# Optimization experiments

Hardware: AMD Instinct MI355X
Metric: run time of the kernel (lower is better)

The kernel has to match this reference:

```python
import jax, jax.numpy as jnp
import numpy as np

# Standard SMPL kinematic tree parents (kintree_table)
PARENTS = np.array([-1, 0, 0, 0, 1, 2, 3, 4, 5, 6, 7, 8, 9, 9, 9,
                    12, 13, 14, 16, 17, 18, 19, 20, 21])
NV, NJ, NB, NP = 6890, 24, 10, 207


def rodrigues(r):
    """Axis-angle [N,3] -> rotation matrices [N,3,3] (Rodrigues formula)."""
    theta = jnp.linalg.norm(r, axis=1, keepdims=True) + 1e-8  # [N,1]
    rh = r / theta                                            # [N,3]
    cos = jnp.cos(theta)[..., None]                           # [N,1,1]
    sin = jnp.sin(theta)[..., None]
    z = jnp.zeros_like(rh[:, 0])
    m = jnp.stack([z, -rh[:, 2], rh[:, 1],
                   rh[:, 2], z, -rh[:, 0],
                   -rh[:, 1], rh[:, 0], z], axis=1).reshape(-1, 3, 3)
    dot = rh[:, :, None] * rh[:, None, :]                     # outer product
    eye = jnp.eye(3, dtype=r.dtype)
    return cos * eye + (1.0 - cos) * dot + sin * m


def setup_inputs() -> dict:
    key = jax.random.key(0)
    ks = jax.random.split(key, 9)
    B = 512
    betas = jax.random.normal(ks[0], (B, NB), dtype=jnp.float32)
    thetas = jax.random.normal(ks[1], (B, NJ * 3), dtype=jnp.float32) * 0.3
    trans = jax.random.normal(ks[2], (B, 3), dtype=jnp.float32)
    scale = jnp.ones((1,), dtype=jnp.float32)
    v_template = jax.random.normal(ks[3], (NV, 3), dtype=jnp.float32)
    shapedirs = jax.random.normal(ks[4], (NV, 3, NB), dtype=jnp.float32) * 0.01
    posedirs = jax.random.normal(ks[5], (NV, 3, NP), dtype=jnp.float32) * 0.01
    Jr = jax.random.uniform(ks[6], (NJ, NV), dtype=jnp.float32)
    J_regressor = Jr / jnp.sum(Jr, axis=1, keepdims=True)
    w = jax.random.uniform(ks[7], (NV, NJ), dtype=jnp.float32)
    weights = w / jnp.sum(w, axis=1, keepdims=True)
    return {"betas": betas, "thetas": thetas, "trans": trans, "scale": scale,
            "v_template": v_template, "shapedirs": shapedirs,
            "posedirs": posedirs, "J_regressor": J_regressor,
            "weights": weights}


def reference(betas, thetas, trans, scale, v_template, shapedirs, posedirs,
              J_regressor, weights):
    B = betas.shape[0]
    dt = betas.dtype
    # Shape blend shapes: v_shaped [B, 6890, 3]
    v_shaped = jnp.einsum('bs,vcs->bvc', betas, shapedirs) + v_template
    # Rest-pose joints J(beta): [B, 24, 3]
    J = jnp.einsum('jv,bvc->bjc', J_regressor, v_shaped)
    # Local rotations from axis-angle, root scaled by `scale`
    lRs = rodrigues(thetas.reshape(-1, 3)).reshape(B, NJ, 3, 3)
    lRs = lRs.at[:, 0].multiply(scale[0])
    # Local joint offsets: root keeps J[:,0], children use J[i] - J[parent[i]]
    parents = jnp.asarray(PARENTS)
    t = J - J[:, jnp.clip(parents, 0)]
    t = t.at[:, 0].set(J[:, 0])
    # Local 4x4 transforms [B, 24, 4, 4]
    top = jnp.concatenate([lRs, t[..., None]], axis=3)          # [B,24,3,4]
    bottom = jnp.broadcast_to(jnp.array([0., 0., 0., 1.], dtype=dt),
                              (B, NJ, 1, 4))
    A = jnp.concatenate([top, bottom], axis=2)
    # Kinematic chain accumulation (fixed 24-joint tree)
    results = [A[:, 0]]
    for i in range(1, NJ):
        results.append(results[PARENTS[i]] @ A[:, i])
    stacked = jnp.stack(results, axis=1)                         # [B,24,4,4]
    # Remove rest-pose joint locations from translation column
    Jh = jnp.concatenate([J, jnp.zeros((B, NJ, 1), dtype=dt)], axis=2)
    deformed = jnp.einsum('bjxy,bjy->bjx', stacked, Jh)          # [B,24,4]
    G = stacked.at[..., 3].add(-deformed)
    # Pose blend shapes from non-root rotations
    lrotmin = (lRs[:, 1:] - jnp.eye(3, dtype=dt)).reshape(B, -1)  # [B,207]
    v_posed = v_shaped + jnp.einsum('bp,vcp->bvc', lrotmin, posedirs)
    # Linear blend skinning
    T = jnp.einsum('bjxy,vj->bvxy', G, weights)                  # [B,6890,4,4]
    vh = jnp.concatenate([v_posed, jnp.ones((B, NV, 1), dtype=dt)], axis=2)
    v = jnp.einsum('bvxy,bvy->bvx', T, vh)[:, :, :3]
    result = v + trans[:, None, :]
    joints = jnp.einsum('jv,bvc->bjc', J_regressor, result)
    return result, joints
```

## Files before the change

kernel.cpp:

```cpp
#include <hip/hip_runtime.h>

#define NVERT 6890
#define NJNT  24
#define NBETA 10
#define NPOSE 207
#define NBATCH 512
#define KPAD 224
#define MROWS 20736
#define NVC (NVERT * 3)

typedef __attribute__((ext_vector_type(8))) short short8;
typedef __attribute__((ext_vector_type(4))) float floatx4;

__constant__ int c_par[NJNT]   = {-1,0,0,0,1,2,3,4,5,6,7,8,9,9,9,12,13,14,16,17,18,19,20,21};
__constant__ int c_depth[NJNT] = { 0,1,1,1,2,2,2,3,3,3,4,4,4,4,4,5,5,5,6,6,7,7,8,8};

static __device__ __forceinline__ unsigned short f2bf(float x) {
  union { float f; unsigned u; } v; v.f = x;
  unsigned r = (v.u + 0x7FFFu + ((v.u >> 16) & 1u)) >> 16;
  return (unsigned short)r;
}
static __device__ __forceinline__ float bf2f(unsigned short h) {
  union { unsigned u; float f; } v; v.u = (unsigned)h << 16;
  return v.f;
}

__global__ __launch_bounds__(256) void k_buildA(
    const float* __restrict__ pdir, const float* __restrict__ sd,
    const float* __restrict__ vt, unsigned short* __restrict__ AT) {
  const int idx = blockIdx.x * 256 + threadIdx.x;
  const int row = idx / KPAD, k = idx - row * KPAD;
  float val = 0.f;
  if (row < NVC) {
    if (k < NPOSE)            val = pdir[(size_t)row * NPOSE + k];
    else if (k < NPOSE + 10)  val = sd[(size_t)row * 10 + (k - NPOSE)];
    else if (k == NPOSE + 10) val = vt[row];
  }
  AT[idx] = f2bf(val);
}

__global__ __launch_bounds__(256) void k_buildW(
    const float* __restrict__ wgt, unsigned short* __restrict__ W16) {
  const int idx = blockIdx.x * 256 + threadIdx.x;
  const int v = idx >> 6, c = idx & 63, j = c & 31, h = c >> 5;
  const float w = (v < NVERT && j < 24) ? wgt[(size_t)v * 24 + j] : 0.f;
  const unsigned short hi = f2bf(w);
  W16[idx] = h ? f2bf(w - bf2f(hi)) : hi;
}

__global__ __launch_bounds__(256) void k_jreg1(
    const float* __restrict__ Jr, const float* __restrict__ vt,
    const float* __restrict__ sd, float* __restrict__ wsJP) {
  const int jc = blockIdx.x, j = jc / 3, c = jc % 3;
  const int v0 = blockIdx.y * 864;
  const int vend = min(NVERT, v0 + 864);
  const int tid = threadIdx.x;
  float acc[11];
  #pragma unroll
  for (int k = 0; k < 11; ++k) acc[k] = 0.f;
  for (int v = v0 + tid; v < vend; v += 256) {
    const float w = Jr[j * NVERT + v];
    acc[0] += w * vt[v * 3 + c];
    const float* s = sd + (size_t)v * 30 + c * 10;
    #pragma unroll
    for (int k = 0; k < 10; ++k) acc[1 + k] += w * s[k];
  }
  #pragma unroll
  for (int off = 32; off > 0; off >>= 1) {
    #pragma unroll
    for (int k = 0; k < 11; ++k) acc[k] += __shfl_down(acc[k], off, 64);
  }
  __shared__ float red[4][11];
  const int lane = tid & 63, wv = tid >> 6;
  if (lane == 0) {
    #pragma unroll
    for (int k = 0; k < 11; ++k) red[wv][k] = acc[k];
  }
  __syncthreads();
  if (tid == 0) {
    #pragma unroll
    for (int k = 0; k < 11; ++k)
      wsJP[(size_t)(blockIdx.y * 72 + jc) * 11 + k] =
          red[0][k] + red[1][k] + red[2][k] + red[3][k];
  }
}

__global__ __launch_bounds__(256, 2) void k_chain3(
    const float* __restrict__ betas, const float* __restrict__ thetas,
    const float* __restrict__ scale, const float* __restrict__ trans,
    const float* __restrict__ wsJP,
    unsigned short* __restrict__ BT, unsigned short* __restrict__ G16) {
  __shared__ __align__(16) float sJ[792];
  __shared__ __align__(16) float sJJ[4][72];
  __shared__ __align__(16) float sM[4][288];
  __shared__ __align__(16) unsigned short sG[4][1024];
  __shared__ __align__(16) unsigned short sB[4][KPAD];

  const int tid = threadIdx.x;
  const int wv = tid >> 6, lane = tid & 63;
  const int b = blockIdx.x * 4 + wv;

  if (tid < 72) {
    #pragma unroll
    for (int k = 0; k < 11; ++k) {
      float s = 0.f;
      #pragma unroll
      for (int c8 = 0; c8 < 8; ++c8) s += wsJP[(size_t)(c8 * 72 + tid) * 11 + k];
      if (k == 0) sJ[tid] = s;
      else        sJ[72 + tid * 10 + (k - 1)] = s;
    }
  }
  #pragma unroll
  for (int r = 0; r < 4; ++r) {
    sG[wv][lane * 16 + r * 4 + 0] = 0; sG[wv][lane * 16 + r * 4 + 1] = 0;
    sG[wv][lane * 16 + r * 4 + 2] = 0; sG[wv][lane * 16 + r * 4 + 3] = 0;
  }
  __syncthreads();

  float R[9], t[3], M[12], Jx = 0.f, Jy = 0.f, Jz = 0.f;
  const int i = lane;
  if (i < NJNT) {
    #pragma unroll
    for (int c = 0; c < 3; ++c) {
      float a = sJ[i * 3 + c];
      const float* d = sJ + 72 + (i * 3 + c) * 10;
      #pragma unroll
      for (int s = 0; s < NBETA; ++s) a += d[s] * betas[b * NBETA + s];
      if (c == 0) Jx = a; else if (c == 1) Jy = a; else Jz = a;
    }
    sJJ[wv][i * 3 + 0] = Jx; sJJ[wv][i * 3 + 1] = Jy; sJJ[wv][i * 3 + 2] = Jz;
    const float rx = thetas[b * 72 + i * 3 + 0];
    const float ry = thetas[b * 72 + i * 3 + 1];
    const float rz = thetas[b * 72 + i * 3 + 2];
    const float th = sqrtf(rx * rx + ry * ry + rz * rz) + 1e-8f;
    const float inv = 1.f / th;
    const float x = rx * inv, y = ry * inv, z = rz * inv;
    const float cs = cosf(th), sn = sinf(th), omc = 1.f - cs;
    R[0] = cs + omc * x * x;     R[1] = omc * x * y - sn * z; R[2] = omc * x * z + sn * y;
    R[3] = omc * x * y + sn * z; R[4] = cs + omc * y * y;     R[5] = omc * y * z - sn * x;
    R[6] = omc * x * z - sn * y; R[7] = omc * y * z + sn * x; R[8] = cs + omc * z * z;
    if (i == 0) {
      const float sc = scale[0];
      #pragma unroll
      for (int k = 0; k < 9; ++k) R[k] *= sc;
    } else {
      #pragma unroll
      for (int k = 0; k < 9; ++k)
        sB[wv][(i - 1) * 9 + k] = f2bf(R[k] - ((k == 0 || k == 4 || k == 8) ? 1.f : 0.f));
    }
  }
  if (i == 0) {
    #pragma unroll
    for (int s = 0; s < NBETA; ++s) sB[wv][NPOSE + s] = f2bf(betas[b * NBETA + s]);
    sB[wv][NPOSE + 10] = 0x3F80;
    #pragma unroll
    for (int k = NPOSE + 11; k < KPAD; ++k) sB[wv][k] = 0;
  }
  __syncthreads();

  if (i < NJNT) {
    if (i == 0) { t[0] = Jx; t[1] = Jy; t[2] = Jz; }
    else {
      const int p = c_par[i];
      t[0] = Jx - sJJ[wv][p * 3 + 0];
      t[1] = Jy - sJJ[wv][p * 3 + 1];
      t[2] = Jz - sJJ[wv][p * 3 + 2];
    }
    if (i == 0) {
      #pragma unroll
      for (int r = 0; r < 3; ++r) {
        M[r*4+0] = R[r*3+0]; M[r*4+1] = R[r*3+1]; M[r*4+2] = R[r*3+2]; M[r*4+3] = t[r];
      }
      #pragma unroll
      for (int k = 0; k < 12; ++k) sM[wv][k] = M[k];
    }
  }
  __syncthreads();

  for (int lvl = 1; lvl <= 8; ++lvl) {
    if (i < NJNT && c_depth[i] == lvl) {
      const float* Mp = sM[wv] + c_par[i] * 12;
      #pragma unroll
      for (int r = 0; r < 3; ++r) {
        const float p0 = Mp[r*4+0], p1 = Mp[r*4+1], p2 = Mp[r*4+2], p3 = Mp[r*4+3];
        M[r*4+0] = p0*R[0] + p1*R[3] + p2*R[6];
        M[r*4+1] = p0*R[1] + p1*R[4] + p2*R[7];
        M[r*4+2] = p0*R[2] + p1*R[5] + p2*R[8];
        M[r*4+3] = p0*t[0] + p1*t[1] + p2*t[2] + p3;
      }
      #pragma unroll
      for (int k = 0; k < 12; ++k) sM[wv][i * 12 + k] = M[k];
    }
    __syncthreads();
  }

  if (i < NJNT) {
    #pragma unroll
    for (int r = 0; r < 3; ++r) {
      M[r*4+3] = M[r*4+3] - (M[r*4+0]*Jx + M[r*4+1]*Jy + M[r*4+2]*Jz)
               + trans[b * 3 + r];
    }
    #pragma unroll
    for (int e = 0; e < 12; ++e) {
      const float g = M[e];
      const unsigned short hi = f2bf(g);
      sG[wv][e * 32 + i]       = hi;
      sG[wv][512 + e * 32 + i] = f2bf(g - bf2f(hi));
    }
  }
  __syncthreads();

  *(uint4*)(G16 + (size_t)b * 1024 + lane * 16)     = *(uint4*)&sG[wv][lane * 16];
  *(uint4*)(G16 + (size_t)b * 1024 + lane * 16 + 8) = *(uint4*)&sG[wv][lane * 16 + 8];
  if (lane < 28)
    *(uint4*)(BT + (size_t)b * KPAD + lane * 8) = *(uint4*)&sB[wv][lane * 8];
}

__global__ __launch_bounds__(256, 3) void k_skin4(
    const unsigned short* __restrict__ AT, const unsigned short* __restrict__ BT,
    const unsigned short* __restrict__ W16, const unsigned short* __restrict__ G16,
    float* __restrict__ out) {
  __shared__ __align__(16) char smem[43776];
  unsigned short* sAs = (unsigned short*)smem;
  unsigned short* sBs = (unsigned short*)(smem + 15360);
  float* sV           = (float*)smem;
  unsigned short* sG2 = (unsigned short*)(smem + 13056);
  unsigned short* sWh = (unsigned short*)(smem + 33536);
  unsigned short* sWl = (unsigned short*)(smem + 38656);

  const int tid = threadIdx.x;
  const int wv = tid >> 6, lane = tid & 63;
  const int q = lane >> 4, n = lane & 15;
  const int b0 = blockIdx.x * 64;
  const int vc0 = blockIdx.y * 192;

  for (int i = tid; i < 512; i += 256) {
    const int row = i >> 3, c8 = i & 7;
    const uint4 w = *(const uint4*)(W16 + (size_t)(blockIdx.y * 64 + row) * 64 + c8 * 8);
    if (c8 < 4) *(uint4*)(sWh + row * 40 + c8 * 8) = w;
    else        *(uint4*)(sWl + row * 40 + (c8 - 4) * 8) = w;
  }

  floatx4 acc[3][4];
  #pragma unroll
  for (int mt = 0; mt < 3; ++mt)
    #pragma unroll
    for (int nt = 0; nt < 4; ++nt) acc[mt][nt] = (floatx4)(0.f);

  const int srow = tid >> 2, sj = tid & 3;
  for (int kt = 0; kt < 7; ++kt) {
    if (kt) __syncthreads();
    #pragma unroll
    for (int it = 0; it < 3; ++it) {
      const int row = it * 64 + srow;
      *(uint4*)(sAs + row * 40 + sj * 8) =
          *(const uint4*)(AT + (size_t)(vc0 + row) * KPAD + kt * 32 + sj * 8);
    }
    *(uint4*)(sBs + srow * 40 + sj * 8) =
        *(const uint4*)(BT + (size_t)(b0 + srow) * KPAD + kt * 32 + sj * 8);
    __syncthreads();
    short8 af[3], bfr[4];
    #pragma unroll
    for (int mt = 0; mt < 3; ++mt)
      af[mt] = *(const short8*)(sAs + (48 * wv + 16 * mt + n) * 40 + q * 8);
    #pragma unroll
    for (int nt = 0; nt < 4; ++nt)
      bfr[nt] = *(const short8*)(sBs + (16 * nt + n) * 40 + q * 8);
    #pragma unroll
    for (int mt = 0; mt < 3; ++mt)
      #pragma unroll
      for (int nt = 0; nt < 4; ++nt)
        acc[mt][nt] = __builtin_amdgcn_mfma_f32_16x16x32_bf16(
            af[mt], bfr[nt], acc[mt][nt], 0, 0, 0);
  }

  short8 wh[4], wl[4];
  #pragma unroll
  for (int vt = 0; vt < 4; ++vt) {
    wh[vt] = *(const short8*)(sWh + (vt * 16 + n) * 40 + q * 8);
    wl[vt] = *(const short8*)(sWl + (vt * 16 + n) * 40 + q * 8);
  }

  for (int nt = 0; nt < 4; ++nt) {
    for (int s = 0; s < 2; ++s) {
      __syncthreads();
      if (s == 0) {
        #pragma unroll
        for (int mt = 0; mt < 3; ++mt)
          #pragma unroll
          for (int r = 0; r < 4; ++r)
            sV[(48 * wv + 16 * mt + 4 * q + r) * 17 + n] = acc[mt][nt][r];
      }
      const int bg0 = b0 + nt * 16 + s * 8;
      for (int i = tid; i < 1024; i += 256) {
        const int row = i >> 2, c4 = i & 3;
        const int t = row >> 5, rem = row & 31;
        *(uint4*)(sG2 + row * 40 + c4 * 8) =
            *(const uint4*)(G16 + (size_t)(bg0 + t) * 1024 + rem * 32 + c4 * 8);
      }
      __syncthreads();
      #pragma unroll
      for (int bb = 0; bb < 2; ++bb) {
        const int t = wv * 2 + bb;
        const int col = s * 8 + t;
        const int bg = b0 + nt * 16 + col;
        const short8 gh = *(const short8*)(sG2 + (t * 32 + n) * 40 + q * 8);
        const short8 gl = *(const short8*)(sG2 + (t * 32 + 16 + n) * 40 + q * 8);
        #pragma unroll
        for (int vt = 0; vt < 4; ++vt) {
          floatx4 a2 = (floatx4)(0.f);
          a2 = __builtin_amdgcn_mfma_f32_16x16x32_bf16(gh, wl[vt], a2, 0, 0, 0);
          a2 = __builtin_amdgcn_mfma_f32_16x16x32_bf16(gl, wh[vt], a2, 0, 0, 0);
          a2 = __builtin_amdgcn_mfma_f32_16x16x32_bf16(gh, wh[vt], a2, 0, 0, 0);
          const float X = sV[(48 * vt + 3 * n + 0) * 17 + col];
          const float Y = sV[(48 * vt + 3 * n + 1) * 17 + col];
          const float Z = sV[(48 * vt + 3 * n + 2) * 17 + col];
          const float o = a2[0] * X + a2[1] * Y + a2[2] * Z + a2[3];
          const int vc = vc0 + 48 * vt + 3 * n + q;
          if (q < 3 && vc < NVC)
            out[(size_t)bg * NVC + vc] = o;
        }
      }
    }
  }
}

__global__ __launch_bounds__(256) void k_joints(
    const float* __restrict__ Jr, const float* __restrict__ res,
    float* __restrict__ joints) {
  const int b = blockIdx.x;
  const int lane = threadIdx.x & 63, wv = threadIdx.x >> 6;
  float acc[18];
  #pragma unroll
  for (int k = 0; k < 18; ++k) acc[k] = 0.f;
  const float* rb = res + (size_t)b * NVC;
  for (int v = lane; v < NVERT; v += 64) {
    const float r0 = rb[v*3+0], r1 = rb[v*3+1], r2 = rb[v*3+2];
    #pragma unroll
    for (int k = 0; k < 6; ++k) {
      const int j = wv + 4 * k;
      const float w = Jr[j * NVERT + v];
      acc[k*3+0] += w * r0; acc[k*3+1] += w * r1; acc[k*3+2] += w * r2;
    }
  }
  #pragma unroll
  for (int off = 32; off > 0; off >>= 1) {
    #pragma unroll
    for (int k = 0; k < 18; ++k) acc[k] += __shfl_down(acc[k], off, 64);
  }
  if (lane == 0) {
    #pragma unroll
    for (int k = 0; k < 6; ++k) {
      const int j = wv + 4 * k;
      joints[(size_t)b * 72 + j * 3 + 0] = acc[k*3+0];
      joints[(size_t)b * 72 + j * 3 + 1] = acc[k*3+1];
      joints[(size_t)b * 72 + j * 3 + 2] = acc[k*3+2];
    }
  }
}

extern "C" void kernel_launch(void* const* d_in, const int* in_sizes, int n_in,
                              void* d_out, int out_size, void* d_ws, size_t ws_size,
                              hipStream_t stream) {
  const float* betas  = (const float*)d_in[0];
  const float* thetas = (const float*)d_in[1];
  const float* trans  = (const float*)d_in[2];
  const float* scale  = (const float*)d_in[3];
  const float* vtpl   = (const float*)d_in[4];
  const float* sd     = (const float*)d_in[5];
  const float* pdir   = (const float*)d_in[6];
  const float* Jr     = (const float*)d_in[7];
  const float* wgt    = (const float*)d_in[8];
  float* out = (float*)d_out;

  float* ws   = (float*)d_ws;
  float* wsJP = ws;
  unsigned short* AT  = (unsigned short*)(ws + 6336);
  unsigned short* BT  = AT + (size_t)MROWS * KPAD;
  unsigned short* W16 = BT + (size_t)NBATCH * KPAD;
  unsigned short* G16 = W16 + (size_t)6912 * 64;

  k_buildA<<<(MROWS * KPAD) / 256, 256, 0, stream>>>(pdir, sd, vtpl, AT);
  k_buildW<<<(6912 * 64) / 256, 256, 0, stream>>>(wgt, W16);
  k_jreg1<<<dim3(72, 8), 256, 0, stream>>>(Jr, vtpl, sd, wsJP);
  k_chain3<<<NBATCH / 4, 256, 0, stream>>>(betas, thetas, scale, trans, wsJP, BT, G16);
  k_skin4<<<dim3(8, 108), 256, 0, stream>>>(AT, BT, W16, G16, out);
  k_joints<<<NBATCH, 256, 0, stream>>>(Jr, out, out + (size_t)NBATCH * NVC);
}
```

Before: 204.9 us.

## Fuse all stages into one cooperative persistent kernel with grid syncs

Replaces the six separate kernel launches with a single cooperative kernel of 256 blocks that runs the four phases (precompute, kinematic chain, skinning GEMM, joint regression) separated by grid-wide syncs. It also removes the two-level joint-regressor partial reduction, since each of 72 blocks now reduces over all vertices, and vectorises the bf16 conversion stores. The aim is to cut launch and inter-kernel gap overhead. In exchange, phase 3 runs on a fixed grid of 256 blocks looping over 864 tiles, phase 2 uses only 128 blocks, and the 72-block regressor reduction is serial over 6890 vertices. A fallback path launches the phases as separate kernels if the cooperative launch fails.

```diff
diff --git a/kernel.cpp b/kernel.cpp
--- a/kernel.cpp
+++ b/kernel.cpp
@@ -1,4 +1,7 @@
 #include <hip/hip_runtime.h>
+#include <hip/hip_cooperative_groups.h>
+
+namespace cg = cooperative_groups;
 
 #define NVERT 6890
 #define NJNT  24
@@ -8,6 +11,7 @@
 #define KPAD 224
 #define MROWS 20736
 #define NVC (NVERT * 3)
+#define GRID 256
 
 typedef __attribute__((ext_vector_type(8))) short short8;
 typedef __attribute__((ext_vector_type(4))) float floatx4;
@@ -25,96 +29,98 @@
   return v.f;
 }
 
-__global__ __launch_bounds__(256) void k_buildA(
-    const float* __restrict__ pdir, const float* __restrict__ sd,
-    const float* __restrict__ vt, unsigned short* __restrict__ AT) {
-  const int idx = blockIdx.x * 256 + threadIdx.x;
-  const int row = idx / KPAD, k = idx - row * KPAD;
-  float val = 0.f;
-  if (row < NVC) {
-    if (k < NPOSE)            val = pdir[(size_t)row * NPOSE + k];
-    else if (k < NPOSE + 10)  val = sd[(size_t)row * 10 + (k - NPOSE)];
-    else if (k == NPOSE + 10) val = vt[row];
-  }
-  AT[idx] = f2bf(val);
-}
-
-__global__ __launch_bounds__(256) void k_buildW(
-    const float* __restrict__ wgt, unsigned short* __restrict__ W16) {
-  const int idx = blockIdx.x * 256 + threadIdx.x;
-  const int v = idx >> 6, c = idx & 63, j = c & 31, h = c >> 5;
-  const float w = (v < NVERT && j < 24) ? wgt[(size_t)v * 24 + j] : 0.f;
-  const unsigned short hi = f2bf(w);
-  W16[idx] = h ? f2bf(w - bf2f(hi)) : hi;
-}
-
-__global__ __launch_bounds__(256) void k_jreg1(
-    const float* __restrict__ Jr, const float* __restrict__ vt,
-    const float* __restrict__ sd, float* __restrict__ wsJP) {
-  const int jc = blockIdx.x, j = jc / 3, c = jc % 3;
-  const int v0 = blockIdx.y * 864;
-  const int vend = min(NVERT, v0 + 864);
+static __device__ __forceinline__ void phase1(
+    const float* __restrict__ Jr, const float* __restrict__ vtpl,
+    const float* __restrict__ sd, const float* __restrict__ pdir,
+    const float* __restrict__ wgt, float* __restrict__ wsJ,
+    unsigned short* __restrict__ AT, unsigned short* __restrict__ W16,
+    char* smem) {
   const int tid = threadIdx.x;
-  float acc[11];
-  #pragma unroll
-  for (int k = 0; k < 11; ++k) acc[k] = 0.f;
-  for (int v = v0 + tid; v < vend; v += 256) {
-    const float w = Jr[j * NVERT + v];
-    acc[0] += w * vt[v * 3 + c];
-    const float* s = sd + (size_t)v * 30 + c * 10;
-    #pragma unroll
-    for (int k = 0; k < 10; ++k) acc[1 + k] += w * s[k];
-  }
-  #pragma unroll
-  for (int off = 32; off > 0; off >>= 1) {
-    #pragma unroll
-    for (int k = 0; k < 11; ++k) acc[k] += __shfl_down(acc[k], off, 64);
-  }
-  __shared__ float red[4][11];
+  const int bid = blockIdx.x;
   const int lane = tid & 63, wv = tid >> 6;
-  if (lane == 0) {
-    #pragma unroll
-    for (int k = 0; k < 11; ++k) red[wv][k] = acc[k];
-  }
-  __syncthreads();
-  if (tid == 0) {
-    #pragma unroll
-    for (int k = 0; k < 11; ++k)
-      wsJP[(size_t)(blockIdx.y * 72 + jc) * 11 + k] =
-          red[0][k] + red[1][k] + red[2][k] + red[3][k];
-  }
-}
-
-__global__ __launch_bounds__(256, 2) void k_chain3(
+  if (bid < 72) {
+    const int j = bid / 3, c = bid - j * 3;
+    float acc[11];
+    #pragma unroll
+    for (int k = 0; k < 11; ++k) acc[k] = 0.f;
+    for (int v = tid; v < NVERT; v += 256) {
+      const float w = Jr[j * NVERT + v];
+      acc[0] += w * vtpl[v * 3 + c];
+      const float* s = sd + (size_t)v * 30 + c * 10;
+      #pragma unroll
+      for (int k = 0; k < 10; ++k) acc[1 + k] += w * s[k];
+    }
+    #pragma unroll
+    for (int off = 32; off > 0; off >>= 1) {
+      #pragma unroll
+      for (int k = 0; k < 11; ++k) acc[k] += __shfl_down(acc[k], off, 64);
+    }
+    float* red = (float*)smem;
+    if (lane == 0) {
+      #pragma unroll
+      for (int k = 0; k < 11; ++k) red[wv * 11 + k] = acc[k];
+    }
+    __syncthreads();
+    if (tid == 0) {
+      #pragma unroll
+      for (int k = 0; k < 11; ++k) {
+        const float s = red[k] + red[11 + k] + red[22 + k] + red[33 + k];
+        if (k == 0) wsJ[bid] = s;
+        else        wsJ[72 + bid * 10 + (k - 1)] = s;
+      }
+    }
+  }
+  const int gid = bid * 256 + tid;
+  const int gstride = gridDim.x * 256;
+  for (int u = gid; u < MROWS * KPAD / 8; u += gstride) {
+    const int row = u / 28, k0 = (u - row * 28) * 8;
+    short8 r;
+    #pragma unroll
+    for (int e = 0; e < 8; ++e) {
+      const int k = k0 + e;
+      float val = 0.f;
+      if (row < NVC) {
+        if (k < NPOSE)            val = pdir[(size_t)row * NPOSE + k];
+        else if (k < NPOSE + 10)  val = sd[(size_t)row * 10 + (k - NPOSE)];
+        else if (k == NPOSE + 10) val = vtpl[row];
+      }
+      r[e] = (short)f2bf(val);
+    }
+    *(short8*)(AT + (size_t)u * 8) = r;
+  }
+  for (int u = gid; u < 6912 * 64 / 8; u += gstride) {
+    const int v = u >> 3, c0 = (u & 7) * 8;
+    short8 r;
+    #pragma unroll
+    for (int e = 0; e < 8; ++e) {
+      const int c = c0 + e, j = c & 31;
+      const float w = (v < NVERT && j < 24) ? wgt[(size_t)v * 24 + j] : 0.f;
+      const unsigned short hi = f2bf(w);
+      r[e] = (short)((c >> 5) ? f2bf(w - bf2f(hi)) : hi);
+    }
+    *(short8*)(W16 + (size_t)u * 8) = r;
+  }
+}
+
+static __device__ __forceinline__ void phase2(
     const float* __restrict__ betas, const float* __restrict__ thetas,
     const float* __restrict__ scale, const float* __restrict__ trans,
-    const float* __restrict__ wsJP,
-    unsigned short* __restrict__ BT, unsigned short* __restrict__ G16) {
-  __shared__ __align__(16) float sJ[792];
-  __shared__ __align__(16) float sJJ[4][72];
-  __shared__ __align__(16) float sM[4][288];
-  __shared__ __align__(16) unsigned short sG[4][1024];
-  __shared__ __align__(16) unsigned short sB[4][KPAD];
-
+    const float* __restrict__ wsJ,
+    unsigned short* __restrict__ BT, unsigned short* __restrict__ G16,
+    char* smem) {
+  if (blockIdx.x >= NBATCH / 4) return;
+  float* sJ  = (float*)smem;
+  float* sJJ = (float*)(smem + 3168);
+  float* sM  = (float*)(smem + 4320);
+  unsigned short* sGc = (unsigned short*)(smem + 8928);
+  unsigned short* sBc = (unsigned short*)(smem + 17120);
   const int tid = threadIdx.x;
   const int wv = tid >> 6, lane = tid & 63;
   const int b = blockIdx.x * 4 + wv;
 
-  if (tid < 72) {
-    #pragma unroll
-    for (int k = 0; k < 11; ++k) {
-      float s = 0.f;
-      #pragma unroll
-      for (int c8 = 0; c8 < 8; ++c8) s += wsJP[(size_t)(c8 * 72 + tid) * 11 + k];
-      if (k == 0) sJ[tid] = s;
-      else        sJ[72 + tid * 10 + (k - 1)] = s;
-    }
-  }
+  for (int i = tid; i < 792; i += 256) sJ[i] = wsJ[i];
   #pragma unroll
-  for (int r = 0; r < 4; ++r) {
-    sG[wv][lane * 16 + r * 4 + 0] = 0; sG[wv][lane * 16 + r * 4 + 1] = 0;
-    sG[wv][lane * 16 + r * 4 + 2] = 0; sG[wv][lane * 16 + r * 4 + 3] = 0;
-  }
+  for (int r = 0; r < 16; ++r) sGc[wv * 1024 + lane * 16 + r] = 0;
   __syncthreads();
 
   float R[9], t[3], M[12], Jx = 0.f, Jy = 0.f, Jz = 0.f;
@@ -128,7 +134,9 @@
       for (int s = 0; s < NBETA; ++s) a += d[s] * betas[b * NBETA + s];
       if (c == 0) Jx = a; else if (c == 1) Jy = a; else Jz = a;
     }
-    sJJ[wv][i * 3 + 0] = Jx; sJJ[wv][i * 3 + 1] = Jy; sJJ[wv][i * 3 + 2] = Jz;
+    sJJ[wv * 72 + i * 3 + 0] = Jx;
+    sJJ[wv * 72 + i * 3 + 1] = Jy;
+    sJJ[wv * 72 + i * 3 + 2] = Jz;
     const float rx = thetas[b * 72 + i * 3 + 0];
     const float ry = thetas[b * 72 + i * 3 + 1];
     const float rz = thetas[b * 72 + i * 3 + 2];
@@ -136,9 +144,9 @@
     const float inv = 1.f / th;
     const float x = rx * inv, y = ry * inv, z = rz * inv;
     const float cs = cosf(th), sn = sinf(th), omc = 1.f - cs;
-    R[0] = cs + omc * x * x;     R[1] = omc * x * y - sn * z; R[2] = omc * x * z + sn * y;
-    R[3] = omc * x * y + sn * z; R[4] = cs + omc * y * y;     R[5] = omc * y * z - sn * x;
-    R[6] = omc * x * z - sn * y; R[7] = omc * y * z + sn * x; R[8] = cs + omc * z * z;
+    R[0] = cs + omc*x*x;   R[1] = omc*x*y - sn*z; R[2] = omc*x*z + sn*y;
+    R[3] = omc*x*y + sn*z; R[4] = cs + omc*y*y;   R[5] = omc*y*z - sn*x;
+    R[6] = omc*x*z - sn*y; R[7] = omc*y*z + sn*x; R[8] = cs + omc*z*z;
     if (i == 0) {
       const float sc = scale[0];
       #pragma unroll
@@ -146,15 +154,17 @@
     } else {
       #pragma unroll
       for (int k = 0; k < 9; ++k)
-        sB[wv][(i - 1) * 9 + k] = f2bf(R[k] - ((k == 0 || k == 4 || k == 8) ? 1.f : 0.f));
+        sBc[wv * 224 + (i - 1) * 9 + k] =
+            f2bf(R[k] - ((k == 0 || k == 4 || k == 8) ? 1.f : 0.f));
     }
   }
   if (i == 0) {
     #pragma unroll
-    for (int s = 0; s < NBETA; ++s) sB[wv][NPOSE + s] = f2bf(betas[b * NBETA + s]);
-    sB[wv][NPOSE + 10] = 0x3F80;
-    #pragma unroll
-    for (int k = NPOSE + 11; k < KPAD; ++k) sB[wv][k] = 0;
+    for (int s = 0; s < NBETA; ++s)
+      sBc[wv * 224 + NPOSE + s] = f2bf(betas[b * NBETA + s]);
+    sBc[wv * 224 + NPOSE + 10] = 0x3F80;
+    #pragma unroll
+    for (int k = NPOSE + 11; k < KPAD; ++k) sBc[wv * 224 + k] = 0;
   }
   __syncthreads();
 
@@ -162,24 +172,25 @@
     if (i == 0) { t[0] = Jx; t[1] = Jy; t[2] = Jz; }
     else {
       const int p = c_par[i];
-      t[0] = Jx - sJJ[wv][p * 3 + 0];
-      t[1] = Jy - sJJ[wv][p * 3 + 1];
-      t[2] = Jz - sJJ[wv][p * 3 + 2];
+      t[0] = Jx - sJJ[wv * 72 + p * 3 + 0];
+      t[1] = Jy - sJJ[wv * 72 + p * 3 + 1];
+      t[2] = Jz - sJJ[wv * 72 + p * 3 + 2];
     }
     if (i == 0) {
       #pragma unroll
       for (int r = 0; r < 3; ++r) {
-        M[r*4+0] = R[r*3+0]; M[r*4+1] = R[r*3+1]; M[r*4+2] = R[r*3+2]; M[r*4+3] = t[r];
-      }
-      #pragma unroll
-      for (int k = 0; k < 12; ++k) sM[wv][k] = M[k];
+        M[r*4+0] = R[r*3+0]; M[r*4+1] = R[r*3+1];
+        M[r*4+2] = R[r*3+2]; M[r*4+3] = t[r];
+      }
+      #pragma unroll
+      for (int k = 0; k < 12; ++k) sM[wv * 288 + k] = M[k];
     }
   }
   __syncthreads();
 
   for (int lvl = 1; lvl <= 8; ++lvl) {
     if (i < NJNT && c_depth[i] == lvl) {
-      const float* Mp = sM[wv] + c_par[i] * 12;
+      const float* Mp = sM + wv * 288 + c_par[i] * 12;
       #pragma unroll
       for (int r = 0; r < 3; ++r) {
         const float p0 = Mp[r*4+0], p1 = Mp[r*4+1], p2 = Mp[r*4+2], p3 = Mp[r*4+3];
@@ -189,7 +200,7 @@
         M[r*4+3] = p0*t[0] + p1*t[1] + p2*t[2] + p3;
       }
       #pragma unroll
-      for (int k = 0; k < 12; ++k) sM[wv][i * 12 + k] = M[k];
+      for (int k = 0; k < 12; ++k) sM[wv * 288 + i * 12 + k] = M[k];
     }
     __syncthreads();
   }
@@ -204,23 +215,25 @@
     for (int e = 0; e < 12; ++e) {
       const float g = M[e];
       const unsigned short hi = f2bf(g);
-      sG[wv][e * 32 + i]       = hi;
-      sG[wv][512 + e * 32 + i] = f2bf(g - bf2f(hi));
+      sGc[wv * 1024 + e * 32 + i]       = hi;
+      sGc[wv * 1024 + 512 + e * 32 + i] = f2bf(g - bf2f(hi));
     }
   }
   __syncthreads();
 
-  *(uint4*)(G16 + (size_t)b * 1024 + lane * 16)     = *(uint4*)&sG[wv][lane * 16];
-  *(uint4*)(G16 + (size_t)b * 1024 + lane * 16 + 8) = *(uint4*)&sG[wv][lane * 16 + 8];
+  *(uint4*)(G16 + (size_t)b * 1024 + lane * 16) =
+      *(uint4*)&sGc[wv * 1024 + lane * 16];
+  *(uint4*)(G16 + (size_t)b * 1024 + lane * 16 + 8) =
+      *(uint4*)&sGc[wv * 1024 + lane * 16 + 8];
   if (lane < 28)
-    *(uint4*)(BT + (size_t)b * KPAD + lane * 8) = *(uint4*)&sB[wv][lane * 8];
-}
-
-__global__ __launch_bounds__(256, 3) void k_skin4(
+    *(uint4*)(BT + (size_t)b * KPAD + lane * 8) =
+        *(uint4*)&sBc[wv * 224 + lane * 8];
+}
+
+static __device__ __forceinline__ void phase3(
     const unsigned short* __restrict__ AT, const unsigned short* __restrict__ BT,
     const unsigned short* __restrict__ W16, const unsigned short* __restrict__ G16,
-    float* __restrict__ out) {
-  __shared__ __align__(16) char smem[43776];
+    float* __restrict__ out, char* smem) {
   unsigned short* sAs = (unsigned short*)smem;
   unsigned short* sBs = (unsigned short*)(smem + 15360);
   float* sV           = (float*)smem;
@@ -231,132 +244,186 @@
   const int tid = threadIdx.x;
   const int wv = tid >> 6, lane = tid & 63;
   const int q = lane >> 4, n = lane & 15;
-  const int b0 = blockIdx.x * 64;
-  const int vc0 = blockIdx.y * 192;
-
-  for (int i = tid; i < 512; i += 256) {
-    const int row = i >> 3, c8 = i & 7;
-    const uint4 w = *(const uint4*)(W16 + (size_t)(blockIdx.y * 64 + row) * 64 + c8 * 8);
-    if (c8 < 4) *(uint4*)(sWh + row * 40 + c8 * 8) = w;
-    else        *(uint4*)(sWl + row * 40 + (c8 - 4) * 8) = w;
-  }
-
-  floatx4 acc[3][4];
-  #pragma unroll
-  for (int mt = 0; mt < 3; ++mt)
-    #pragma unroll
-    for (int nt = 0; nt < 4; ++nt) acc[mt][nt] = (floatx4)(0.f);
-
-  const int srow = tid >> 2, sj = tid & 3;
-  for (int kt = 0; kt < 7; ++kt) {
-    if (kt) __syncthreads();
-    #pragma unroll
-    for (int it = 0; it < 3; ++it) {
-      const int row = it * 64 + srow;
-      *(uint4*)(sAs + row * 40 + sj * 8) =
-          *(const uint4*)(AT + (size_t)(vc0 + row) * KPAD + kt * 32 + sj * 8);
-    }
-    *(uint4*)(sBs + srow * 40 + sj * 8) =
-        *(const uint4*)(BT + (size_t)(b0 + srow) * KPAD + kt * 32 + sj * 8);
+
+  for (int tile = blockIdx.x; tile < 864; tile += gridDim.x) {
     __syncthreads();
-    short8 af[3], bfr[4];
+    const int b0 = (tile & 7) * 64;
+    const int vty = tile >> 3;
+    const int vc0 = vty * 192;
+
+    for (int i = tid; i < 512; i += 256) {
+      const int row = i >> 3, c8 = i & 7;
+      const uint4 w = *(const uint4*)(W16 + (size_t)(vty * 64 + row) * 64 + c8 * 8);
+      if (c8 < 4) *(uint4*)(sWh + row * 40 + c8 * 8) = w;
+      else        *(uint4*)(sWl + row * 40 + (c8 - 4) * 8) = w;
+    }
+
+    floatx4 acc[3][4];
     #pragma unroll
     for (int mt = 0; mt < 3; ++mt)
-      af[mt] = *(const short8*)(sAs + (48 * wv + 16 * mt + n) * 40 + q * 8);
-    #pragma unroll
-    for (int nt = 0; nt < 4; ++nt)
-      bfr[nt] = *(const short8*)(sBs + (16 * nt + n) * 40 + q * 8);
-    #pragma unroll
-    for (int mt = 0; mt < 3; ++mt)
+      #pragma unroll
+      for (int nt = 0; nt < 4; ++nt) acc[mt][nt] = (floatx4)(0.f);
+
+    const int srow = tid >> 2, sj = tid & 3;
+    for (int kt = 0; kt < 7; ++kt) {
+      if (kt) __syncthreads();
+      #pragma unroll
+      for (int it = 0; it < 3; ++it) {
+        const int row = it * 64 + srow;
+        *(uint4*)(sAs + row * 40 + sj * 8) =
+            *(const uint4*)(AT + (size_t)(vc0 + row) * KPAD + kt * 32 + sj * 8);
+      }
+      *(uint4*)(sBs + srow * 40 + sj * 8) =
+          *(const uint4*)(BT + (size_t)(b0 + srow) * KPAD + kt * 32 + sj * 8);
+      __syncthreads();
+      short8 af[3], bfr[4];
+      #pragma unroll
+      for (int mt = 0; mt < 3; ++mt)
+        af[mt] = *(const short8*)(sAs + (48 * wv + 16 * mt + n) * 40 + q * 8);
       #pragma unroll
       for (int nt = 0; nt < 4; ++nt)
-        acc[mt][nt] = __builtin_amdgcn_mfma_f32_16x16x32_bf16(
-            af[mt], bfr[nt], acc[mt][nt], 0, 0, 0);
-  }
-
-  short8 wh[4], wl[4];
-  #pragma unroll
-  for (int vt = 0; vt < 4; ++vt) {
-    wh[vt] = *(const short8*)(sWh + (vt * 16 + n) * 40 + q * 8);
-    wl[vt] = *(const short8*)(sWl + (vt * 16 + n) * 40 + q * 8);
-  }
-
-  for (int nt = 0; nt < 4; ++nt) {
-    for (int s = 0; s < 2; ++s) {
-      __syncthreads();
-      if (s == 0) {
+        bfr[nt] = *(const short8*)(sBs + (16 * nt + n) * 40 + q * 8);
+      #pragma unroll
+      for (int mt = 0; mt < 3; ++mt)
         #pragma unroll
-        for (int mt = 0; mt < 3; ++mt)
+        for (int nt = 0; nt < 4; ++nt)
+          acc[mt][nt] = __builtin_amdgcn_mfma_f32_16x16x32_bf16(
+              af[mt], bfr[nt], acc[mt][nt], 0, 0, 0);
+    }
+
+    short8 wh[4], wl[4];
+    #pragma unroll
+    for (int vt = 0; vt < 4; ++vt) {
+      wh[vt] = *(const short8*)(sWh + (vt * 16 + n) * 40 + q * 8);
+      wl[vt] = *(const short8*)(sWl + (vt * 16 + n) * 40 + q * 8);
+    }
+
+    for (int nt = 0; nt < 4; ++nt) {
+      for (int s = 0; s < 2; ++s) {
+        __syncthreads();
+        if (s == 0) {
           #pragma unroll
-          for (int r = 0; r < 4; ++r)
-            sV[(48 * wv + 16 * mt + 4 * q + r) * 17 + n] = acc[mt][nt][r];
-      }
-      const int bg0 = b0 + nt * 16 + s * 8;
-      for (int i = tid; i < 1024; i += 256) {
-        const int row = i >> 2, c4 = i & 3;
-        const int t = row >> 5, rem = row & 31;
-        *(uint4*)(sG2 + row * 40 + c4 * 8) =
-            *(const uint4*)(G16 + (size_t)(bg0 + t) * 1024 + rem * 32 + c4 * 8);
-      }
-      __syncthreads();
-      #pragma unroll
-      for (int bb = 0; bb < 2; ++bb) {
-        const int t = wv * 2 + bb;
-        const int col = s * 8 + t;
-        const int bg = b0 + nt * 16 + col;
-        const short8 gh = *(const short8*)(sG2 + (t * 32 + n) * 40 + q * 8);
-        const short8 gl = *(const short8*)(sG2 + (t * 32 + 16 + n) * 40 + q * 8);
+          for (int mt = 0; mt < 3; ++mt)
+            #pragma unroll
+            for (int r = 0; r < 4; ++r)
+              sV[(48 * wv + 16 * mt + 4 * q + r) * 17 + n] = acc[mt][nt][r];
+        }
+        const int bg0 = b0 + nt * 16 + s * 8;
+        for (int i = tid; i < 1024; i += 256) {
+          const int row = i >> 2, c4 = i & 3;
+          const int t = row >> 5, rem = row & 31;
+          *(uint4*)(sG2 + row * 40 + c4 * 8) =
+              *(const uint4*)(G16 + (size_t)(bg0 + t) * 1024 + rem * 32 + c4 * 8);
+        }
+        __syncthreads();
         #pragma unroll
-        for (int vt = 0; vt < 4; ++vt) {
-          floatx4 a2 = (floatx4)(0.f);
-          a2 = __builtin_amdgcn_mfma_f32_16x16x32_bf16(gh, wl[vt], a2, 0, 0, 0);
-          a2 = __builtin_amdgcn_mfma_f32_16x16x32_bf16(gl, wh[vt], a2, 0, 0, 0);
-          a2 = __builtin_amdgcn_mfma_f32_16x16x32_bf16(gh, wh[vt], a2, 0, 0, 0);
-          const float X = sV[(48 * vt + 3 * n + 0) * 17 + col];
-          const float Y = sV[(48 * vt + 3 * n + 1) * 17 + col];
-          const float Z = sV[(48 * vt + 3 * n + 2) * 17 + col];
-          const float o = a2[0] * X + a2[1] * Y + a2[2] * Z + a2[3];
-          const int vc = vc0 + 48 * vt + 3 * n + q;
-          if (q < 3 && vc < NVC)
-            out[(size_t)bg * NVC + vc] = o;
+        for (int bb = 0; bb < 2; ++bb) {
+          const int t = wv * 2 + bb;
+          const int col = s * 8 + t;
+          const int bg = b0 + nt * 16 + col;
+          const short8 gh = *(const short8*)(sG2 + (t * 32 + n) * 40 + q * 8);
+          const short8 gl = *(const short8*)(sG2 + (t * 32 + 16 + n) * 40 + q * 8);
+          #pragma unroll
+          for (int vt = 0; vt < 4; ++vt) {
+            floatx4 a2 = (floatx4)(0.f);
+            a2 = __builtin_amdgcn_mfma_f32_16x16x32_bf16(gh, wl[vt], a2, 0, 0, 0);
+            a2 = __builtin_amdgcn_mfma_f32_16x16x32_bf16(gl, wh[vt], a2, 0, 0, 0);
+            a2 = __builtin_amdgcn_mfma_f32_16x16x32_bf16(gh, wh[vt], a2, 0, 0, 0);
+            const float X = sV[(48 * vt + 3 * n + 0) * 17 + col];
+            const float Y = sV[(48 * vt + 3 * n + 1) * 17 + col];
+            const float Z = sV[(48 * vt + 3 * n + 2) * 17 + col];
+            const float o = a2[0] * X + a2[1] * Y + a2[2] * Z + a2[3];
+            const int vc = vc0 + 48 * vt + 3 * n + q;
+            if (q < 3 && vc < NVC)
+              out[(size_t)bg * NVC + vc] = o;
+          }
         }
       }
     }
   }
 }
 
-__global__ __launch_bounds__(256) void k_joints(
-    const float* __restrict__ Jr, const float* __restrict__ res,
-    float* __restrict__ joints) {
-  const int b = blockIdx.x;
+static __device__ __forceinline__ void phase4(
+    const float* __restrict__ Jr, float* __restrict__ out) {
   const int lane = threadIdx.x & 63, wv = threadIdx.x >> 6;
-  float acc[18];
-  #pragma unroll
-  for (int k = 0; k < 18; ++k) acc[k] = 0.f;
-  const float* rb = res + (size_t)b * NVC;
-  for (int v = lane; v < NVERT; v += 64) {
-    const float r0 = rb[v*3+0], r1 = rb[v*3+1], r2 = rb[v*3+2];
-    #pragma unroll
-    for (int k = 0; k < 6; ++k) {
-      const int j = wv + 4 * k;
-      const float w = Jr[j * NVERT + v];
-      acc[k*3+0] += w * r0; acc[k*3+1] += w * r1; acc[k*3+2] += w * r2;
-    }
-  }
-  #pragma unroll
-  for (int off = 32; off > 0; off >>= 1) {
-    #pragma unroll
-    for (int k = 0; k < 18; ++k) acc[k] += __shfl_down(acc[k], off, 64);
-  }
-  if (lane == 0) {
-    #pragma unroll
-    for (int k = 0; k < 6; ++k) {
-      const int j = wv + 4 * k;
-      joints[(size_t)b * 72 + j * 3 + 0] = acc[k*3+0];
-      joints[(size_t)b * 72 + j * 3 + 1] = acc[k*3+1];
-      joints[(size_t)b * 72 + j * 3 + 2] = acc[k*3+2];
-    }
-  }
+  float* jout = out + (size_t)NBATCH * NVC;
+  for (int b = blockIdx.x; b < NBATCH; b += gridDim.x) {
+    float jacc[18];
+    #pragma unroll
+    for (int k = 0; k < 18; ++k) jacc[k] = 0.f;
+    const float* rb = out + (size_t)b * NVC;
+    for (int v = lane; v < NVERT; v += 64) {
+      const float r0 = rb[v*3+0], r1 = rb[v*3+1], r2 = rb[v*3+2];
+      #pragma unroll
+      for (int k = 0; k < 6; ++k) {
+        const int j = wv + 4 * k;
+        const float w = Jr[j * NVERT + v];
+        jacc[k*3+0] += w * r0; jacc[k*3+1] += w * r1; jacc[k*3+2] += w * r2;
+      }
+    }
+    #pragma unroll
+    for (int off = 32; off > 0; off >>= 1) {
+      #pragma unroll
+      for (int k = 0; k < 18; ++k) jacc[k] += __shfl_down(jacc[k], off, 64);
+    }
+    if (lane == 0) {
+      #pragma unroll
+      for (int k = 0; k < 6; ++k) {
+        const int j = wv + 4 * k;
+        jout[(size_t)b * 72 + j * 3 + 0] = jacc[k*3+0];
+        jout[(size_t)b * 72 + j * 3 + 1] = jacc[k*3+1];
+        jout[(size_t)b * 72 + j * 3 + 2] = jacc[k*3+2];
+      }
+    }
+  }
+}
+
+__global__ __launch_bounds__(256, 2) void k_mono(
+    const float* __restrict__ betas, const float* __restrict__ thetas,
+    const float* __restrict__ trans, const float* __restrict__ scale,
+    const float* __restrict__ vtpl, const float* __restrict__ sd,
+    const float* __restrict__ pdir, const float* __restrict__ Jr,
+    const float* __restrict__ wgt, float* __restrict__ out,
+    float* __restrict__ wsJ, unsigned short* __restrict__ AT,
+    unsigned short* __restrict__ BT, unsigned short* __restrict__ W16,
+    unsigned short* __restrict__ G16) {
+  __shared__ __align__(16) char smem[44032];
+  cg::grid_group gg = cg::this_grid();
+  phase1(Jr, vtpl, sd, pdir, wgt, wsJ, AT, W16, smem);
+  __threadfence(); gg.sync();
+  phase2(betas, thetas, scale, trans, wsJ, BT, G16, smem);
+  __threadfence(); gg.sync();
+  phase3(AT, BT, W16, G16, out, smem);
+  __threadfence(); gg.sync();
+  phase4(Jr, out);
+}
+
+__global__ __launch_bounds__(256, 2) void k_p1(
+    const float* __restrict__ Jr, const float* __restrict__ vtpl,
+    const float* __restrict__ sd, const float* __restrict__ pdir,
+    const float* __restrict__ wgt, float* __restrict__ wsJ,
+    unsigned short* __restrict__ AT, unsigned short* __restrict__ W16) {
+  __shared__ __align__(16) char smem[192];
+  phase1(Jr, vtpl, sd, pdir, wgt, wsJ, AT, W16, smem);
+}
+__global__ __launch_bounds__(256, 2) void k_p2(
+    const float* __restrict__ betas, const float* __restrict__ thetas,
+    const float* __restrict__ scale, const float* __restrict__ trans,
+    const float* __restrict__ wsJ, unsigned short* __restrict__ BT,
+    unsigned short* __restrict__ G16) {
+  __shared__ __align__(16) char smem[18912];
+  phase2(betas, thetas, scale, trans, wsJ, BT, G16, smem);
+}
+__global__ __launch_bounds__(256, 2) void k_p3(
+    const unsigned short* __restrict__ AT, const unsigned short* __restrict__ BT,
+    const unsigned short* __restrict__ W16, const unsigned short* __restrict__ G16,
+    float* __restrict__ out) {
+  __shared__ __align__(16) char smem[44032];
+  phase3(AT, BT, W16, G16, out, smem);
+}
+__global__ __launch_bounds__(256, 2) void k_p4(
+    const float* __restrict__ Jr, float* __restrict__ out) {
+  phase4(Jr, out);
 }
 
 extern "C" void kernel_launch(void* const* d_in, const int* in_sizes, int n_in,
@@ -373,17 +440,26 @@
   const float* wgt    = (const float*)d_in[8];
   float* out = (float*)d_out;
 
-  float* ws   = (float*)d_ws;
-  float* wsJP = ws;
-  unsigned short* AT  = (unsigned short*)(ws + 6336);
+  float* ws  = (float*)d_ws;
+  float* wsJ = ws;
+  unsigned short* AT  = (unsigned short*)(ws + 792);
   unsigned short* BT  = AT + (size_t)MROWS * KPAD;
   unsigned short* W16 = BT + (size_t)NBATCH * KPAD;
   unsigned short* G16 = W16 + (size_t)6912 * 64;
 
-  k_buildA<<<(MROWS * KPAD) / 256, 256, 0, stream>>>(pdir, sd, vtpl, AT);
-  k_buildW<<<(6912 * 64) / 256, 256, 0, stream>>>(wgt, W16);
-  k_jreg1<<<dim3(72, 8), 256, 0, stream>>>(Jr, vtpl, sd, wsJP);
-  k_chain3<<<NBATCH / 4, 256, 0, stream>>>(betas, thetas, scale, trans, wsJP, BT, G16);
-  k_skin4<<<dim3(8, 108), 256, 0, stream>>>(AT, BT, W16, G16, out);
-  k_joints<<<NBATCH, 256, 0, stream>>>(Jr, out, out + (size_t)NBATCH * NVC);
-}
+  void* args[] = {
+    (void*)&betas, (void*)&thetas, (void*)&trans, (void*)&scale,
+    (void*)&vtpl, (void*)&sd, (void*)&pdir, (void*)&Jr, (void*)&wgt,
+    (void*)&out, (void*)&wsJ, (void*)&AT, (void*)&BT, (void*)&W16,
+    (void*)&G16
+  };
+  hipError_t err = hipLaunchCooperativeKernel(
+      reinterpret_cast<void*>(k_mono), dim3(GRID), dim3(256), args, 0, stream);
+  if (err != hipSuccess) {
+    (void)hipGetLastError();
+    k_p1<<<256, 256, 0, stream>>>(Jr, vtpl, sd, pdir, wgt, wsJ, AT, W16);
+    k_p2<<<128, 256, 0, stream>>>(betas, thetas, scale, trans, wsJ, BT, G16);
+    k_p3<<<864, 256, 0, stream>>>(AT, BT, W16, G16, out);
+    k_p4<<<512, 256, 0, stream>>>(Jr, out);
+  }
+}
```

Result: slower. 456.9 us (+123.0%).
